# Performance work log

Hardware: AMD Instinct MI355X
Metric: run time of the kernel (lower is better)

Reference implementation:

```python
import jax, jax.numpy as jnp
import numpy as np
import math

H_SP, W_SP = 200, 200          # BEV spatial shape (single level, m == h)
D_MODEL = 256
N_HEADS = 8
N_POINTS = 4
D_HEAD = D_MODEL // N_HEADS


def _grid_init_bias():
    # Matches TemporalSelfAttention._reset_parameters for sampling_offsets.bias
    thetas = np.arange(N_HEADS, dtype=np.float32) * (2.0 * np.pi / N_HEADS)
    grid = np.stack([np.cos(thetas), np.sin(thetas)], -1)
    grid = grid / np.abs(grid).max(-1, keepdims=True)
    grid = np.tile(grid[:, None, None, :], (1, 1, N_POINTS, 1))  # (NH, 1, P, 2)
    for i in range(N_POINTS):
        grid[:, :, i, :] *= (i + 1)
    return jnp.asarray(grid.reshape(-1), dtype=jnp.float32)


def setup_inputs() -> dict:
    key = jax.random.key(0)
    ks = jax.random.split(key, 10)
    N = 1
    Lq = H_SP * W_SP
    Lin = H_SP * W_SP
    xav = math.sqrt(6.0 / (2 * D_MODEL))
    query = jax.random.normal(ks[0], (N, Lq, D_MODEL), jnp.float32)
    query_pos = jax.random.normal(ks[1], (N, Lq, D_MODEL), jnp.float32)
    reference_points = jax.random.uniform(ks[2], (N, Lq, 1, 2), jnp.float32)
    input_flatten = jax.random.normal(ks[3], (N, Lin, D_MODEL), jnp.float32)
    W_value = jax.random.uniform(ks[4], (D_MODEL, D_MODEL), jnp.float32, -xav, xav)
    b_value = jnp.zeros((D_MODEL,), jnp.float32)
    # small random weights (trained-model-like) + canonical grid bias
    W_off = jax.random.normal(ks[5], (N_HEADS * N_POINTS * 2, D_MODEL), jnp.float32) * 0.005
    b_off = _grid_init_bias()
    W_attn = jax.random.normal(ks[6], (N_HEADS * N_POINTS, D_MODEL), jnp.float32) * 0.02
    b_attn = jnp.zeros((N_HEADS * N_POINTS,), jnp.float32)
    W_out = jax.random.uniform(ks[7], (D_MODEL, D_MODEL), jnp.float32, -xav, xav)
    b_out = jnp.zeros((D_MODEL,), jnp.float32)
    return dict(query=query, query_pos=query_pos, reference_points=reference_points,
                input_flatten=input_flatten, W_value=W_value, b_value=b_value,
                W_off=W_off, b_off=b_off, W_attn=W_attn, b_attn=b_attn,
                W_out=W_out, b_out=b_out)


def _bilinear_sample(vflat, x, y):
    # vflat: (N, NH, H*W, DH); x, y: (N, NH, K) pixel coords (align_corners=False)
    # Zero padding outside the feature map, matching the MSDeformAttn CUDA kernel.
    x0f = jnp.floor(x)
    y0f = jnp.floor(y)
    x0 = x0f.astype(jnp.int32)
    y0 = y0f.astype(jnp.int32)
    lw = x - x0f
    lh = y - y0f
    gather = jax.vmap(jax.vmap(lambda v, i: v[i]))  # over batch, head
    acc = jnp.zeros(x.shape + (vflat.shape[-1],), vflat.dtype)
    corners = ((y0, x0, (1.0 - lh) * (1.0 - lw)),
               (y0, x0 + 1, (1.0 - lh) * lw),
               (y0 + 1, x0, lh * (1.0 - lw)),
               (y0 + 1, x0 + 1, lh * lw))
    for yi, xi, wgt in corners:
        valid = ((xi >= 0) & (xi < W_SP) & (yi >= 0) & (yi < H_SP)).astype(vflat.dtype)
        idx = jnp.clip(yi, 0, H_SP - 1) * W_SP + jnp.clip(xi, 0, W_SP - 1)
        g = gather(vflat, idx)                      # (N, NH, K, DH)
        acc = acc + (wgt * valid)[..., None] * g
    return acc


def reference(query, query_pos, reference_points, input_flatten,
              W_value, b_value, W_off, b_off, W_attn, b_attn, W_out, b_out):
    N, Lq, _ = query.shape
    q = query + query_pos
    value = input_flatten @ W_value.T + b_value                     # (N, Lin, D)
    value = value.reshape(N, -1, N_HEADS, D_HEAD).transpose(0, 2, 1, 3)  # (N, NH, Lin, DH)
    off = (q @ W_off.T + b_off).reshape(N, Lq, N_HEADS, N_POINTS, 2)
    attn = jax.nn.softmax((q @ W_attn.T + b_attn).reshape(N, Lq, N_HEADS, N_POINTS), axis=-1)
    norm = jnp.array([W_SP, H_SP], jnp.float32)                      # offset_normalizer (w, h)
    ref = reference_points[:, :, 0, :][:, :, None, None, :]          # (N, Lq, 1, 1, 2)
    loc = ref + off / norm                                           # (N, Lq, NH, P, 2) in [0,1]
    x = (loc[..., 0] * W_SP - 0.5).transpose(0, 2, 1, 3).reshape(N, N_HEADS, Lq * N_POINTS)
    y = (loc[..., 1] * H_SP - 0.5).transpose(0, 2, 1, 3).reshape(N, N_HEADS, Lq * N_POINTS)
    sampled = _bilinear_sample(value, x, y).reshape(N, N_HEADS, Lq, N_POINTS, D_HEAD)
    out = jnp.einsum('nhqpd,nqhp->nqhd', sampled, attn).reshape(N, Lq, D_MODEL)
    return out @ W_out.T + b_out
```

## Files before the change

### kernel.cpp

```cpp
#include <hip/hip_runtime.h>
#include <math.h>

#define LQ 40000
#define DMODEL 256
#define NHD 8
#define NPT 4
#define DHD 32
#define HSP 200
#define WSP 200

typedef short s16x8 __attribute__((ext_vector_type(8)));
typedef float f32x4 __attribute__((ext_vector_type(4)));

__device__ __forceinline__ unsigned short f2b(float f) {
    unsigned u = __builtin_bit_cast(unsigned, f);
    u += 0x7FFFu + ((u >> 16) & 1u);
    return (unsigned short)(u >> 16);
}
__device__ __forceinline__ float b2f(unsigned short u) {
    return __builtin_bit_cast(float, ((unsigned)u) << 16);
}
__device__ __forceinline__ void pk8(const float4& v0, const float4& v1,
                                    unsigned short* o) {
    o[0] = f2b(v0.x); o[1] = f2b(v0.y); o[2] = f2b(v0.z); o[3] = f2b(v0.w);
    o[4] = f2b(v1.x); o[5] = f2b(v1.y); o[6] = f2b(v1.z); o[7] = f2b(v1.w);
}


__global__ __launch_bounds__(256) void convert_weights(
    const float* __restrict__ Wv, const float* __restrict__ Woff,
    const float* __restrict__ Wattn, const float* __restrict__ Wout,
    unsigned short* __restrict__ dst)
{
    int u = blockIdx.x * 256 + threadIdx.x;
    int lane = u & 63, ks = (u >> 6) & 7, slot = u >> 9;
    int l15 = lane & 15, quad = lane >> 4;
    const float* src;
    if (slot < 16) {
        src = Wv + (size_t)(slot * 16 + l15) * 256;
    } else if (slot < 22) {
        int col = (slot - 16) * 16 + l15;
        src = (col < 64) ? Woff + (size_t)col * 256
                         : Wattn + (size_t)(col - 64) * 256;
    } else {
        src = Wout + (size_t)((slot - 22) * 16 + l15) * 256;
    }
    int k0 = ks * 32 + quad * 8;
    float4 v0 = *(const float4*)(src + k0);
    float4 v1 = *(const float4*)(src + k0 + 4);
    union { unsigned short u16[8]; uint4 v; } tmp;
    pk8(v0, v1, tmp.u16);
    *(uint4*)(dst + (size_t)u * 8) = tmp.v;
}

template <int NT, int TPW, int CMODE, bool HasA2>
__global__ __launch_bounds__(256, 2) void gemm_fused(
    const float* __restrict__ A, const float* __restrict__ A2,
    const unsigned short* __restrict__ Wf,
    const float* __restrict__ b1, const float* __restrict__ b2, int split,
    void* __restrict__ Cv)
{
    const int t = threadIdx.x;
    const int wave = t >> 6, lane = t & 63;
    const int l15 = lane & 15, quad = lane >> 4;

    s16x8 bf[TPW][8];
    float bias[TPW];
#pragma unroll
    for (int j = 0; j < TPW; ++j) {
        bias[j] = 0.f;
        int c = wave * TPW + j;
        if (c < NT) {
#pragma unroll
            for (int ks = 0; ks < 8; ++ks)
                bf[j][ks] = *(const s16x8*)&Wf[(size_t)(c * 8 + ks) * 512 + lane * 8];
            int col = c * 16 + l15;
            bias[j] = (col < split) ? b1[col] : b2[col - split];
        }
    }

#pragma unroll
    for (int s = 0; s < 2; ++s) {
        const size_t g = (size_t)blockIdx.x * 2 + s;
        const size_t rowoff = (g * 16 + l15) * 256;
        s16x8 a[8];
#pragma unroll
        for (int ks = 0; ks < 8; ++ks) {
            int k0 = ks * 32 + quad * 8;
            float4 v0 = *(const float4*)(A + rowoff + k0);
            float4 v1 = *(const float4*)(A + rowoff + k0 + 4);
            if constexpr (HasA2) {
                float4 w0 = *(const float4*)(A2 + rowoff + k0);
                float4 w1 = *(const float4*)(A2 + rowoff + k0 + 4);
                v0.x += w0.x; v0.y += w0.y; v0.z += w0.z; v0.w += w0.w;
                v1.x += w1.x; v1.y += w1.y; v1.z += w1.z; v1.w += w1.w;
            }
            union { unsigned short u16[8]; s16x8 v; } tmp;
            pk8(v0, v1, tmp.u16);
            a[ks] = tmp.v;
        }
#pragma unroll
        for (int j = 0; j < TPW; ++j) {
            int c = wave * TPW + j;
            if (c < NT) {
                f32x4 acc = (f32x4){0.f, 0.f, 0.f, 0.f};
#pragma unroll
                for (int ks = 0; ks < 8; ++ks)
                    acc = __builtin_amdgcn_mfma_f32_16x16x32_bf16(a[ks], bf[j][ks],
                                                                  acc, 0, 0, 0);
#pragma unroll
                for (int r2 = 0; r2 < 4; ++r2) {
                    size_t row = g * 16 + quad * 4 + r2;
                    float v = acc[r2] + bias[j];
                    if constexpr (CMODE == 1) {
                        ((unsigned short*)Cv)[(((size_t)(c >> 1) * LQ + row) << 5)
                                              + ((c & 1) << 4) + l15] = f2b(v);
                    } else if constexpr (CMODE == 2) {
                        int col = c * 16 + l15;
                        int hh, jj;
                        if (col < 64) { hh = col >> 3; jj = col & 7; }
                        else          { hh = (col - 64) >> 2; jj = 8 + (col & 3); }
                        ((float*)Cv)[((size_t)hh * LQ + row) * 12 + jj] = v;
                    } else {
                        ((float*)Cv)[row * (NT * 16) + c * 16 + l15] = v;
                    }
                }
            }
        }
    }
}

template <int NT, int TPW>
__global__ __launch_bounds__(256, 2) void gemm_rs(
    const unsigned short* __restrict__ Af, const unsigned short* __restrict__ Wf,
    const float* __restrict__ b1, float* __restrict__ C)
{
    const int t = threadIdx.x;
    const int wave = t >> 6, lane = t & 63;
    const int l15 = lane & 15, quad = lane >> 4;

    s16x8 bf[TPW][8];
    float bias[TPW];
#pragma unroll
    for (int j = 0; j < TPW; ++j) {
        int c = wave * TPW + j;
#pragma unroll
        for (int ks = 0; ks < 8; ++ks)
            bf[j][ks] = *(const s16x8*)&Wf[(size_t)(c * 8 + ks) * 512 + lane * 8];
        bias[j] = b1[c * 16 + l15];
    }

#pragma unroll
    for (int s = 0; s < 2; ++s) {
        const size_t g = (size_t)blockIdx.x * 2 + s;
        s16x8 a[8];
#pragma unroll
        for (int ks = 0; ks < 8; ++ks)
            a[ks] = *(const s16x8*)&Af[g * 4096 + ks * 512 + lane * 8];
#pragma unroll
        for (int j = 0; j < TPW; ++j) {
            int c = wave * TPW + j;
            f32x4 acc = (f32x4){0.f, 0.f, 0.f, 0.f};
#pragma unroll
            for (int ks = 0; ks < 8; ++ks)
                acc = __builtin_amdgcn_mfma_f32_16x16x32_bf16(a[ks], bf[j][ks],
                                                              acc, 0, 0, 0);
#pragma unroll
            for (int r2 = 0; r2 < 4; ++r2) {
                size_t row = g * 16 + quad * 4 + r2;
                C[row * (NT * 16) + c * 16 + l15] = acc[r2] + bias[j];
            }
        }
    }
}

__global__ __launch_bounds__(256) void sample_kernel(
    const float* __restrict__ raw2, const float* __restrict__ rp,
    const unsigned short* __restrict__ value, unsigned short* __restrict__ outa)
{
    __shared__ int4   sIdx[64][4];
    __shared__ float4 sW[64][4];

    const int h = blockIdx.x & 7;
    const int q0 = (blockIdx.x >> 3) * 64;
    const int t = threadIdx.x;
    {
        const int qi = t >> 2, p = t & 3;
        const int q = q0 + qi;
        const float* r = raw2 + ((size_t)h * LQ + q) * 12;
        float l0 = r[8], l1 = r[9], l2 = r[10], l3 = r[11];
        float mx = fmaxf(fmaxf(l0, l1), fmaxf(l2, l3));
        float e0 = __expf(l0 - mx), e1 = __expf(l1 - mx);
        float e2 = __expf(l2 - mx), e3 = __expf(l3 - mx);
        float inv = 1.f / (e0 + e1 + e2 + e3);
        float ep = (p == 0) ? e0 : (p == 1) ? e1 : (p == 2) ? e2 : e3;
        float wp = ep * inv;

        float x = rp[(size_t)q * 2 + 0] * (float)WSP - 0.5f + r[p * 2 + 0];
        float y = rp[(size_t)q * 2 + 1] * (float)HSP - 0.5f + r[p * 2 + 1];
        float x0f = floorf(x), y0f = floorf(y);
        int x0 = (int)x0f, y0 = (int)y0f;
        float lw = x - x0f, lh = y - y0f;
        float cw[4] = {(1.f - lh) * (1.f - lw), (1.f - lh) * lw,
                       lh * (1.f - lw), lh * lw};
        int4 I; float4 W;
        int* Ip = &I.x; float* Wp = &W.x;
#pragma unroll
        for (int c = 0; c < 4; ++c) {
            int cx = x0 + (c & 1), cy = y0 + (c >> 1);
            bool valid = (cx >= 0) & (cx < WSP) & (cy >= 0) & (cy < HSP);
            int ccx = cx < 0 ? 0 : (cx > WSP - 1 ? WSP - 1 : cx);
            int ccy = cy < 0 ? 0 : (cy > HSP - 1 ? HSP - 1 : cy);
            Ip[c] = (ccy * WSP + ccx) * DHD;
            Wp[c] = valid ? cw[c] * wp : 0.f;
        }
        sIdx[qi][p] = I;
        sW[qi][p] = W;
    }
    __syncthreads();

    const int d8 = t & 7, qp = t >> 3;
    const unsigned short* vp = value + (size_t)h * LQ * DHD + d8 * 4;
#pragma unroll
    for (int e = 0; e < 2; ++e) {
        int qi = qp * 2 + e;
        float a0 = 0.f, a1 = 0.f, a2 = 0.f, a3 = 0.f;
#pragma unroll
        for (int p = 0; p < 4; ++p) {
            int4 I = sIdx[qi][p];
            float4 W = sW[qi][p];
            uint2 g0 = *(const uint2*)(vp + I.x);
            uint2 g1 = *(const uint2*)(vp + I.y);
            uint2 g2 = *(const uint2*)(vp + I.z);
            uint2 g3 = *(const uint2*)(vp + I.w);
            a0 += W.x * b2f((unsigned short)g0.x);
            a1 += W.x * b2f((unsigned short)(g0.x >> 16));
            a2 += W.x * b2f((unsigned short)g0.y);
            a3 += W.x * b2f((unsigned short)(g0.y >> 16));
            a0 += W.y * b2f((unsigned short)g1.x);
            a1 += W.y * b2f((unsigned short)(g1.x >> 16));
            a2 += W.y * b2f((unsigned short)g1.y);
            a3 += W.y * b2f((unsigned short)(g1.y >> 16));
            a0 += W.z * b2f((unsigned short)g2.x);
            a1 += W.z * b2f((unsigned short)(g2.x >> 16));
            a2 += W.z * b2f((unsigned short)g2.y);
            a3 += W.z * b2f((unsigned short)(g2.y >> 16));
            a0 += W.w * b2f((unsigned short)g3.x);
            a1 += W.w * b2f((unsigned short)(g3.x >> 16));
            a2 += W.w * b2f((unsigned short)g3.y);
            a3 += W.w * b2f((unsigned short)(g3.y >> 16));
        }
        int q = q0 + qi;
        size_t off = (size_t)(q >> 4) * 4096 + h * 512 + (d8 >> 1) * 128
                   + (q & 15) * 8 + (d8 & 1) * 4;
        union { unsigned short u16[4]; uint2 v; } o;
        o.u16[0] = f2b(a0); o.u16[1] = f2b(a1);
        o.u16[2] = f2b(a2); o.u16[3] = f2b(a3);
        *(uint2*)&outa[off] = o.v;
    }
}

extern "C" void kernel_launch(void* const* d_in, const int* in_sizes, int n_in,
                              void* d_out, int out_size, void* d_ws, size_t ws_size,
                              hipStream_t stream)
{
    const float* query         = (const float*)d_in[0];
    const float* query_pos     = (const float*)d_in[1];
    const float* ref_points    = (const float*)d_in[2];
    const float* input_flatten = (const float*)d_in[3];
    const float* W_value       = (const float*)d_in[4];
    const float* b_value       = (const float*)d_in[5];
    const float* W_off         = (const float*)d_in[6];
    const float* b_off         = (const float*)d_in[7];
    const float* W_attn        = (const float*)d_in[8];
    const float* b_attn        = (const float*)d_in[9];
    const float* W_out         = (const float*)d_in[10];
    const float* b_out         = (const float*)d_in[11];
    float* out = (float*)d_out;

    unsigned short* val  = (unsigned short*)d_ws;
    float*          raw2 = (float*)(val + (size_t)LQ * DMODEL);
    unsigned short* outa = (unsigned short*)(raw2 + (size_t)LQ * 96);
    unsigned short* wf   = outa + (size_t)LQ * DMODEL;
    unsigned short* wfv  = wf;
    unsigned short* wfoa = wf + 65536;
    unsigned short* wfo  = wf + 90112;

    dim3 blk(256);

    convert_weights<<<dim3(76), blk, 0, stream>>>(W_value, W_off, W_attn, W_out, wf);

    gemm_fused<16, 4, 1, false><<<dim3(LQ / 32), blk, 0, stream>>>(
        input_flatten, nullptr, wfv, b_value, b_value, 256, val);

    gemm_fused<6, 2, 2, true><<<dim3(LQ / 32), blk, 0, stream>>>(
        query, query_pos, wfoa, b_off, b_attn, 64, raw2);

    sample_kernel<<<dim3(8 * (LQ / 64)), blk, 0, stream>>>(raw2, ref_points, val, outa);

    gemm_rs<16, 4><<<dim3(LQ / 32), blk, 0, stream>>>(outa, wfo, b_out, out);
}
```

Measured before the change: 259.7 us.

## Merge value and offset GEMMs into one persistent launch with LDS-staged weights

The value-projection and offset/attention-projection GEMMs are combined into a single persistent kernel. Block ranges take different roles: two groups of 128 blocks each compute half of the value columns, and 256 blocks compute the offset/attention columns. Weights are staged once per block into LDS instead of being held in registers, and each wave loops over row strips in a grid-stride fashion. The output GEMM is reworked the same way, with 256 persistent blocks that each cover half the columns. This removes one launch and spreads per-block weight loading over many strips, but the value-GEMM input rows are now read twice (once per column half), and it adds LDS traffic for the B operand.

```diff
diff --git a/kernel.cpp b/kernel.cpp
--- a/kernel.cpp
+++ b/kernel.cpp
@@ -8,6 +8,9 @@
 #define DHD 32
 #define HSP 200
 #define WSP 200
+#define NSTRIP (LQ / 16)
+#define G1B 128
+#define G2B 256
 
 typedef short s16x8 __attribute__((ext_vector_type(8)));
 typedef float f32x4 __attribute__((ext_vector_type(4)));
@@ -53,122 +56,166 @@
     *(uint4*)(dst + (size_t)u * 8) = tmp.v;
 }
 
-template <int NT, int TPW, int CMODE, bool HasA2>
-__global__ __launch_bounds__(256, 2) void gemm_fused(
-    const float* __restrict__ A, const float* __restrict__ A2,
-    const unsigned short* __restrict__ Wf,
-    const float* __restrict__ b1, const float* __restrict__ b2, int split,
-    void* __restrict__ Cv)
-{
+
+__global__ __launch_bounds__(256, 2) void gemm12(
+    const float* __restrict__ input_flatten,
+    const float* __restrict__ query, const float* __restrict__ query_pos,
+    const unsigned short* __restrict__ wf,
+    const float* __restrict__ bv, const float* __restrict__ boff,
+    const float* __restrict__ battn,
+    unsigned short* __restrict__ val, float* __restrict__ raw2)
+{
+    __shared__ unsigned short Blds[32768];
+
+    const int bid = blockIdx.x;
     const int t = threadIdx.x;
+    const int role = (bid < 2 * G1B) ? 0 : 1;
+    const int half8 = (bid >= G1B && role == 0) ? 1 : 0;
+
+    {
+        const uint4* src = (const uint4*)(wf + (role ? 16 : half8 * 8) * 4096);
+        const int nu = role ? 3072 : 4096;
+        for (int i = t; i < nu; i += 256) ((uint4*)Blds)[i] = src[i];
+    }
+    __syncthreads();
+
     const int wave = t >> 6, lane = t & 63;
     const int l15 = lane & 15, quad = lane >> 4;
 
-    s16x8 bf[TPW][8];
-    float bias[TPW];
-#pragma unroll
-    for (int j = 0; j < TPW; ++j) {
-        bias[j] = 0.f;
-        int c = wave * TPW + j;
-        if (c < NT) {
-#pragma unroll
-            for (int ks = 0; ks < 8; ++ks)
-                bf[j][ks] = *(const s16x8*)&Wf[(size_t)(c * 8 + ks) * 512 + lane * 8];
+    if (role == 0) {
+        float bias[8];
+#pragma unroll
+        for (int c = 0; c < 8; ++c) bias[c] = bv[(half8 * 8 + c) * 16 + l15];
+        const int wgid = (bid - half8 * G1B) * 4 + wave;
+        for (int g = wgid; g < NSTRIP; g += G1B * 4) {
+            const float* base = input_flatten + ((size_t)g * 16 + l15) * 256;
+            float4 p0[8], p1[8];
+#pragma unroll
+            for (int ks = 0; ks < 8; ++ks) {
+                p0[ks] = *(const float4*)(base + ks * 32 + quad * 8);
+                p1[ks] = *(const float4*)(base + ks * 32 + quad * 8 + 4);
+            }
+            asm volatile("" ::: "memory");
+            s16x8 a[8];
+#pragma unroll
+            for (int ks = 0; ks < 8; ++ks) {
+                union { unsigned short u16[8]; s16x8 v; } tmp;
+                pk8(p0[ks], p1[ks], tmp.u16);
+                a[ks] = tmp.v;
+            }
+#pragma unroll
+            for (int c = 0; c < 8; ++c) {
+                const int gc = half8 * 8 + c;
+                f32x4 acc = (f32x4){0.f, 0.f, 0.f, 0.f};
+#pragma unroll
+                for (int ks = 0; ks < 8; ++ks)
+                    acc = __builtin_amdgcn_mfma_f32_16x16x32_bf16(
+                        a[ks], *(const s16x8*)&Blds[c * 4096 + ks * 512 + lane * 8],
+                        acc, 0, 0, 0);
+#pragma unroll
+                for (int r2 = 0; r2 < 4; ++r2) {
+                    size_t row = (size_t)g * 16 + quad * 4 + r2;
+                    val[(((size_t)(gc >> 1) * LQ + row) << 5) + ((gc & 1) << 4) + l15]
+                        = f2b(acc[r2] + bias[c]);
+                }
+            }
+        }
+    } else {
+        float bias[6];
+#pragma unroll
+        for (int c = 0; c < 6; ++c) {
             int col = c * 16 + l15;
-            bias[j] = (col < split) ? b1[col] : b2[col - split];
-        }
-    }
-
-#pragma unroll
-    for (int s = 0; s < 2; ++s) {
-        const size_t g = (size_t)blockIdx.x * 2 + s;
-        const size_t rowoff = (g * 16 + l15) * 256;
-        s16x8 a[8];
-#pragma unroll
-        for (int ks = 0; ks < 8; ++ks) {
-            int k0 = ks * 32 + quad * 8;
-            float4 v0 = *(const float4*)(A + rowoff + k0);
-            float4 v1 = *(const float4*)(A + rowoff + k0 + 4);
-            if constexpr (HasA2) {
-                float4 w0 = *(const float4*)(A2 + rowoff + k0);
-                float4 w1 = *(const float4*)(A2 + rowoff + k0 + 4);
-                v0.x += w0.x; v0.y += w0.y; v0.z += w0.z; v0.w += w0.w;
-                v1.x += w1.x; v1.y += w1.y; v1.z += w1.z; v1.w += w1.w;
-            }
-            union { unsigned short u16[8]; s16x8 v; } tmp;
-            pk8(v0, v1, tmp.u16);
-            a[ks] = tmp.v;
-        }
-#pragma unroll
-        for (int j = 0; j < TPW; ++j) {
-            int c = wave * TPW + j;
-            if (c < NT) {
+            bias[c] = (col < 64) ? boff[col] : battn[col - 64];
+        }
+        const int wgid = (bid - 2 * G1B) * 4 + wave;
+        for (int g = wgid; g < NSTRIP; g += G2B * 4) {
+            const float* base  = query     + ((size_t)g * 16 + l15) * 256;
+            const float* base2 = query_pos + ((size_t)g * 16 + l15) * 256;
+            float4 p0[8], p1[8], q0[8], q1[8];
+#pragma unroll
+            for (int ks = 0; ks < 8; ++ks) {
+                p0[ks] = *(const float4*)(base + ks * 32 + quad * 8);
+                p1[ks] = *(const float4*)(base + ks * 32 + quad * 8 + 4);
+                q0[ks] = *(const float4*)(base2 + ks * 32 + quad * 8);
+                q1[ks] = *(const float4*)(base2 + ks * 32 + quad * 8 + 4);
+            }
+            asm volatile("" ::: "memory");
+            s16x8 a[8];
+#pragma unroll
+            for (int ks = 0; ks < 8; ++ks) {
+                float4 v0 = p0[ks], v1 = p1[ks];
+                v0.x += q0[ks].x; v0.y += q0[ks].y;
+                v0.z += q0[ks].z; v0.w += q0[ks].w;
+                v1.x += q1[ks].x; v1.y += q1[ks].y;
+                v1.z += q1[ks].z; v1.w += q1[ks].w;
+                union { unsigned short u16[8]; s16x8 v; } tmp;
+                pk8(v0, v1, tmp.u16);
+                a[ks] = tmp.v;
+            }
+#pragma unroll
+            for (int c = 0; c < 6; ++c) {
                 f32x4 acc = (f32x4){0.f, 0.f, 0.f, 0.f};
 #pragma unroll
                 for (int ks = 0; ks < 8; ++ks)
-                    acc = __builtin_amdgcn_mfma_f32_16x16x32_bf16(a[ks], bf[j][ks],
-                                                                  acc, 0, 0, 0);
+                    acc = __builtin_amdgcn_mfma_f32_16x16x32_bf16(
+                        a[ks], *(const s16x8*)&Blds[c * 4096 + ks * 512 + lane * 8],
+                        acc, 0, 0, 0);
 #pragma unroll
                 for (int r2 = 0; r2 < 4; ++r2) {
-                    size_t row = g * 16 + quad * 4 + r2;
-                    float v = acc[r2] + bias[j];
-                    if constexpr (CMODE == 1) {
-                        ((unsigned short*)Cv)[(((size_t)(c >> 1) * LQ + row) << 5)
-                                              + ((c & 1) << 4) + l15] = f2b(v);
-                    } else if constexpr (CMODE == 2) {
-                        int col = c * 16 + l15;
-                        int hh, jj;
-                        if (col < 64) { hh = col >> 3; jj = col & 7; }
-                        else          { hh = (col - 64) >> 2; jj = 8 + (col & 3); }
-                        ((float*)Cv)[((size_t)hh * LQ + row) * 12 + jj] = v;
-                    } else {
-                        ((float*)Cv)[row * (NT * 16) + c * 16 + l15] = v;
-                    }
+                    size_t row = (size_t)g * 16 + quad * 4 + r2;
+                    float v = acc[r2] + bias[c];
+                    int col = c * 16 + l15;
+                    int hh, jj;
+                    if (col < 64) { hh = col >> 3; jj = col & 7; }
+                    else          { hh = (col - 64) >> 2; jj = 8 + (col & 3); }
+                    raw2[((size_t)hh * LQ + row) * 12 + jj] = v;
                 }
             }
         }
     }
 }
 
-template <int NT, int TPW>
-__global__ __launch_bounds__(256, 2) void gemm_rs(
-    const unsigned short* __restrict__ Af, const unsigned short* __restrict__ Wf,
-    const float* __restrict__ b1, float* __restrict__ C)
-{
+__global__ __launch_bounds__(256, 2) void gemm4(
+    const unsigned short* __restrict__ Af, const unsigned short* __restrict__ wf,
+    const float* __restrict__ bout, float* __restrict__ C)
+{
+    __shared__ unsigned short Blds[32768];
+
     const int t = threadIdx.x;
+    const int half8 = blockIdx.x >> 7;
+    {
+        const uint4* src = (const uint4*)(wf + (22 + half8 * 8) * 4096);
+        for (int i = t; i < 4096; i += 256) ((uint4*)Blds)[i] = src[i];
+    }
+    __syncthreads();
+
     const int wave = t >> 6, lane = t & 63;
     const int l15 = lane & 15, quad = lane >> 4;
 
-    s16x8 bf[TPW][8];
-    float bias[TPW];
-#pragma unroll
-    for (int j = 0; j < TPW; ++j) {
-        int c = wave * TPW + j;
+    float bias[8];
+#pragma unroll
+    for (int c = 0; c < 8; ++c) bias[c] = bout[(half8 * 8 + c) * 16 + l15];
+
+    const int wgid = (blockIdx.x & 127) * 4 + wave;
+    for (int g = wgid; g < NSTRIP; g += 128 * 4) {
+        s16x8 a[8];
 #pragma unroll
         for (int ks = 0; ks < 8; ++ks)
-            bf[j][ks] = *(const s16x8*)&Wf[(size_t)(c * 8 + ks) * 512 + lane * 8];
-        bias[j] = b1[c * 16 + l15];
-    }
-
-#pragma unroll
-    for (int s = 0; s < 2; ++s) {
-        const size_t g = (size_t)blockIdx.x * 2 + s;
-        s16x8 a[8];
-#pragma unroll
-        for (int ks = 0; ks < 8; ++ks)
-            a[ks] = *(const s16x8*)&Af[g * 4096 + ks * 512 + lane * 8];
-#pragma unroll
-        for (int j = 0; j < TPW; ++j) {
-            int c = wave * TPW + j;
+            a[ks] = *(const s16x8*)&Af[(size_t)g * 4096 + ks * 512 + lane * 8];
+        asm volatile("" ::: "memory");
+#pragma unroll
+        for (int c = 0; c < 8; ++c) {
+            const int gc = half8 * 8 + c;
             f32x4 acc = (f32x4){0.f, 0.f, 0.f, 0.f};
 #pragma unroll
             for (int ks = 0; ks < 8; ++ks)
-                acc = __builtin_amdgcn_mfma_f32_16x16x32_bf16(a[ks], bf[j][ks],
-                                                              acc, 0, 0, 0);
+                acc = __builtin_amdgcn_mfma_f32_16x16x32_bf16(
+                    a[ks], *(const s16x8*)&Blds[c * 4096 + ks * 512 + lane * 8],
+                    acc, 0, 0, 0);
 #pragma unroll
             for (int r2 = 0; r2 < 4; ++r2) {
-                size_t row = g * 16 + quad * 4 + r2;
-                C[row * (NT * 16) + c * 16 + l15] = acc[r2] + bias[j];
+                size_t row = (size_t)g * 16 + quad * 4 + r2;
+                C[row * 256 + gc * 16 + l15] = acc[r2] + bias[c];
             }
         }
     }
@@ -282,21 +329,16 @@
     float*          raw2 = (float*)(val + (size_t)LQ * DMODEL);
     unsigned short* outa = (unsigned short*)(raw2 + (size_t)LQ * 96);
     unsigned short* wf   = outa + (size_t)LQ * DMODEL;
-    unsigned short* wfv  = wf;
-    unsigned short* wfoa = wf + 65536;
-    unsigned short* wfo  = wf + 90112;
 
     dim3 blk(256);
 
     convert_weights<<<dim3(76), blk, 0, stream>>>(W_value, W_off, W_attn, W_out, wf);
 
-    gemm_fused<16, 4, 1, false><<<dim3(LQ / 32), blk, 0, stream>>>(
-        input_flatten, nullptr, wfv, b_value, b_value, 256, val);
-
-    gemm_fused<6, 2, 2, true><<<dim3(LQ / 32), blk, 0, stream>>>(
-        query, query_pos, wfoa, b_off, b_attn, 64, raw2);
+    gemm12<<<dim3(2 * G1B + G2B), blk, 0, stream>>>(
+        input_flatten, query, query_pos, wf,
+        b_value, b_off, b_attn, val, raw2);
 
     sample_kernel<<<dim3(8 * (LQ / 64)), blk, 0, stream>>>(raw2, ref_points, val, outa);
 
-    gemm_rs<16, 4><<<dim3(LQ / 32), blk, 0, stream>>>(outa, wfo, b_out, out);
-}
+    gemm4<<<dim3(256), blk, 0, stream>>>(outa, wf, b_out, out);
+}
```

New measurement: 236.2 us. 1.1x faster.
